# Kernel tuning notes

Hardware: AMD Instinct MI355X
Metric: run time of the kernel (lower is better)

The kernel has to match this reference:

```python
import jax, jax.numpy as jnp
import numpy as np

S, B, D = 2048, 4, 512
H, R, QK, FFN = 8, 8, 32, 2048
HD = D // H  # 64


def _ln(x, g, b, eps=1e-5):
    mu = jnp.mean(x, axis=-1, keepdims=True)
    var = jnp.var(x, axis=-1, keepdims=True)
    return (x - mu) * jax.lax.rsqrt(var + eps) * g + b


def setup_inputs() -> dict:
    key = jax.random.key(0)
    ks = jax.random.split(key, 16)
    w = lambda k, shape: (jax.random.normal(k, shape, jnp.float32) * 0.02)
    return {
        "x": jax.random.normal(ks[0], (S, B, D), jnp.float32),
        "Wq": w(ks[1], (D, D)),        "bq": jnp.zeros((D,), jnp.float32),
        "Wk": w(ks[2], (D, D)),        "bk": jnp.zeros((D,), jnp.float32),
        "Wv": w(ks[3], (D, HD * R)),   "bv": jnp.zeros((HD * R,), jnp.float32),
        "Wqv": w(ks[4], (D, QK * H)),  "bqv": jnp.zeros((QK * H,), jnp.float32),
        "Wkv": w(ks[5], (HD, QK)),     "bkv": jnp.zeros((QK,), jnp.float32),
        "Wf": w(ks[6], (D, D)),        "bf": jnp.zeros((D,), jnp.float32),
        "W1": w(ks[7], (D, FFN)),      "b1": jnp.zeros((FFN,), jnp.float32),
        "W2": w(ks[8], (FFN, D)),      "b2": jnp.zeros((D,), jnp.float32),
        "g1": jnp.ones((D,), jnp.float32),  "be1": jnp.zeros((D,), jnp.float32),
        "g2": jnp.ones((D,), jnp.float32),  "be2": jnp.zeros((D,), jnp.float32),
    }


def reference(x, Wq, bq, Wk, bk, Wv, bv, Wqv, bqv, Wkv, bkv, Wf, bf,
              W1, b1, W2, b2, g1, be1, g2, be2):
    # x: [S, B, D] -> [B, S, D]
    xb = jnp.transpose(x, (1, 0, 2))
    bsz, n, _ = xb.shape
    res = xb

    # stage 1: per-head attention over positions
    q = (xb @ Wq + bq).reshape(bsz, n, H, HD) / np.sqrt(HD).astype(np.float32)
    k = (xb @ Wk + bk).reshape(bsz, n, H, HD)
    v = (xb @ Wv + bv).reshape(bsz, n, R, HD)
    score = jax.nn.softmax(jnp.einsum("bshd,bthd->bhst", q, k), axis=-1)  # [B,H,S,S]
    # retrieved values per (head, rule): [B, S, H, R, HD]
    out = jnp.einsum("bhst,btrd->bshrd", score, v)

    # stage 2: composition softmax over rules
    qv = (xb @ Wqv + bqv).reshape(bsz, n, H, QK) / np.sqrt(QK).astype(np.float32)
    kv = out @ Wkv + bkv  # [B,S,H,R,QK]
    comp = jax.nn.softmax(jnp.einsum("bshq,bshrq->bshr", qv, kv), axis=-1)
    o = jnp.einsum("bshr,bshrd->bshd", comp, out).reshape(bsz, n, D)
    o = o @ Wf + bf

    # post-norm residual + FFN (norm_before=False)
    o = _ln(res + o, g1, be1)
    ffn = jax.nn.relu(o @ W1 + b1) @ W2 + b2
    o = _ln(o + ffn, g2, be2)
    return jnp.transpose(o, (1, 0, 2))  # back to [S, B, D]
```

## Files before the change

### kernel.cpp

```cpp
#include <hip/hip_runtime.h>
#include <hip/hip_bf16.h>

typedef __bf16 bf16;
typedef bf16 bf16x4 __attribute__((ext_vector_type(4)));
typedef bf16 bf16x8 __attribute__((ext_vector_type(8)));
typedef float f32x4 __attribute__((ext_vector_type(4)));

constexpr int SEQ  = 2048;
constexpr int BAT  = 4;
constexpr int NH   = 8;
constexpr int NTOK = SEQ * BAT;
constexpr int QKVW = 1792;
constexpr size_t MB = 1ull << 20;

__device__ inline void async_lds16(const void* g, void* l) {
  __builtin_amdgcn_global_load_lds(
      (__attribute__((address_space(1))) void*)(g),
      (__attribute__((address_space(3))) void*)(l), 16, 0, 0);
}

#define MFMA16 __builtin_amdgcn_mfma_f32_16x16x32_bf16

__global__ __launch_bounds__(512)
void attn_kernel(const bf16* __restrict__ qkv, const bf16* __restrict__ vT,
                 bf16* __restrict__ outb) {
  __shared__ __align__(16) bf16 Qs[64 * 64];
  __shared__ __align__(16) bf16 Ks[2][128 * 64];
  __shared__ __align__(16) bf16 Ps[64 * 128];
  __shared__ float rsAll[8][64];
  __shared__ float rsInv[64];

  const int tid = threadIdx.x;
  const int lane = tid & 63, w = tid >> 6;
  const int r16 = lane & 15, rq = lane >> 4;
  const int qb = blockIdx.x, h = blockIdx.y, b = blockIdx.z;

  const bf16* qbase = qkv + ((long)b * SEQ + qb * 64) * QKVW + h * 64;
  {
    const int rr = tid >> 3, sl = tid & 7;
    async_lds16(qbase + (long)rr * QKVW + ((sl ^ (rr & 7)) << 3),
                Qs + (size_t)w * 512);
  }
  const bf16* kbase = qkv + (long)b * SEQ * QKVW + 512 + h * 64;
  auto stageK = [&](int buf, int t0) {
#pragma unroll
    for (int g = 0; g < 2; g++) {
      const int c = g * 512 + tid;
      const int rr = c >> 3, sl = c & 7;
      async_lds16(kbase + (long)(t0 + rr) * QKVW + ((sl ^ (rr & 7)) << 3),
                  Ks[buf] + (size_t)(g * 8 + w) * 512);
    }
  };
  const bf16* vp[4];
#pragma unroll
  for (int n = 0; n < 4; n++)
    vp[n] = vT + ((long)b * 512 + w * 64 + n * 16 + r16) * SEQ + rq * 8;

  f32x4 acc[4][4] = {};
  float rs[4] = {};

  stageK(0, 0);
  asm volatile("s_waitcnt vmcnt(0)" ::: "memory");
  __builtin_amdgcn_s_barrier();
  __builtin_amdgcn_sched_barrier(0);

  bf16x8 qf[4][2];
#pragma unroll
  for (int j = 0; j < 4; j++)
#pragma unroll
    for (int kf = 0; kf < 2; kf++) {
      const int row = j * 16 + r16;
      qf[j][kf] = *(const bf16x8*)&Qs[row * 64 + (((kf * 4 + rq) ^ (row & 7)) << 3)];
    }

  const int krow = w * 16 + r16;
  for (int t = 0; t < 16; ++t) {
    const int t0 = t * 128;
    if (t) {
      asm volatile("s_waitcnt vmcnt(0)" ::: "memory");
      __builtin_amdgcn_s_barrier();
      __builtin_amdgcn_sched_barrier(0);
    }
    if (t < 15) stageK((t + 1) & 1, t0 + 128);
    bf16x8 va0 = *(const bf16x8*)(vp[0] + t0);
    bf16x8 va1 = *(const bf16x8*)(vp[1] + t0);
    bf16x8 va2 = *(const bf16x8*)(vp[2] + t0);
    bf16x8 va3 = *(const bf16x8*)(vp[3] + t0);
    bf16x8 kfr[2];
#pragma unroll
    for (int kf = 0; kf < 2; kf++)
      kfr[kf] = *(const bf16x8*)&Ks[t & 1][krow * 64 + (((kf * 4 + rq) ^ (krow & 7)) << 3)];
    f32x4 s[4] = {};
#pragma unroll
    for (int j = 0; j < 4; j++) {
      s[j] = MFMA16(kfr[0], qf[j][0], s[j], 0, 0, 0);
      s[j] = MFMA16(kfr[1], qf[j][1], s[j], 0, 0, 0);
    }
#pragma unroll
    for (int j = 0; j < 4; j++) {
      const float e0 = __expf(s[j][0]), e1 = __expf(s[j][1]);
      const float e2 = __expf(s[j][2]), e3 = __expf(s[j][3]);
      rs[j] += (e0 + e1) + (e2 + e3);
      bf16x4 pk; pk[0] = (bf16)e0; pk[1] = (bf16)e1; pk[2] = (bf16)e2; pk[3] = (bf16)e3;
      const int row = j * 16 + r16;
      *(bf16x4*)&Ps[row * 128 + (((w * 2 + (rq >> 1)) ^ (row & 7)) << 3) + ((rq & 1) << 2)] = pk;
    }
    asm volatile("s_waitcnt lgkmcnt(0)" ::: "memory");
    __builtin_amdgcn_s_barrier();
    __builtin_amdgcn_sched_barrier(0);
    bf16x8 pf[4];
#pragma unroll
    for (int i = 0; i < 4; i++) {
      const int row = i * 16 + r16;
      pf[i] = *(const bf16x8*)&Ps[row * 128 + (((rq + 0) ^ (row & 7)) << 3)];
    }
    bf16x8 vb0 = *(const bf16x8*)(vp[0] + t0 + 32);
    bf16x8 vb1 = *(const bf16x8*)(vp[1] + t0 + 32);
    bf16x8 vb2 = *(const bf16x8*)(vp[2] + t0 + 32);
    bf16x8 vb3 = *(const bf16x8*)(vp[3] + t0 + 32);
#pragma unroll
    for (int i = 0; i < 4; i++) {
      acc[i][0] = MFMA16(pf[i], va0, acc[i][0], 0, 0, 0);
      acc[i][1] = MFMA16(pf[i], va1, acc[i][1], 0, 0, 0);
      acc[i][2] = MFMA16(pf[i], va2, acc[i][2], 0, 0, 0);
      acc[i][3] = MFMA16(pf[i], va3, acc[i][3], 0, 0, 0);
    }
#pragma unroll
    for (int i = 0; i < 4; i++) {
      const int row = i * 16 + r16;
      pf[i] = *(const bf16x8*)&Ps[row * 128 + (((rq + 4) ^ (row & 7)) << 3)];
    }
    va0 = *(const bf16x8*)(vp[0] + t0 + 64);
    va1 = *(const bf16x8*)(vp[1] + t0 + 64);
    va2 = *(const bf16x8*)(vp[2] + t0 + 64);
    va3 = *(const bf16x8*)(vp[3] + t0 + 64);
#pragma unroll
    for (int i = 0; i < 4; i++) {
      acc[i][0] = MFMA16(pf[i], vb0, acc[i][0], 0, 0, 0);
      acc[i][1] = MFMA16(pf[i], vb1, acc[i][1], 0, 0, 0);
      acc[i][2] = MFMA16(pf[i], vb2, acc[i][2], 0, 0, 0);
      acc[i][3] = MFMA16(pf[i], vb3, acc[i][3], 0, 0, 0);
    }
#pragma unroll
    for (int i = 0; i < 4; i++) {
      const int row = i * 16 + r16;
      pf[i] = *(const bf16x8*)&Ps[row * 128 + (((rq + 8) ^ (row & 7)) << 3)];
    }
    vb0 = *(const bf16x8*)(vp[0] + t0 + 96);
    vb1 = *(const bf16x8*)(vp[1] + t0 + 96);
    vb2 = *(const bf16x8*)(vp[2] + t0 + 96);
    vb3 = *(const bf16x8*)(vp[3] + t0 + 96);
#pragma unroll
    for (int i = 0; i < 4; i++) {
      acc[i][0] = MFMA16(pf[i], va0, acc[i][0], 0, 0, 0);
      acc[i][1] = MFMA16(pf[i], va1, acc[i][1], 0, 0, 0);
      acc[i][2] = MFMA16(pf[i], va2, acc[i][2], 0, 0, 0);
      acc[i][3] = MFMA16(pf[i], va3, acc[i][3], 0, 0, 0);
    }
#pragma unroll
    for (int i = 0; i < 4; i++) {
      const int row = i * 16 + r16;
      pf[i] = *(const bf16x8*)&Ps[row * 128 + (((rq + 12) ^ (row & 7)) << 3)];
    }
#pragma unroll
    for (int i = 0; i < 4; i++) {
      acc[i][0] = MFMA16(pf[i], vb0, acc[i][0], 0, 0, 0);
      acc[i][1] = MFMA16(pf[i], vb1, acc[i][1], 0, 0, 0);
      acc[i][2] = MFMA16(pf[i], vb2, acc[i][2], 0, 0, 0);
      acc[i][3] = MFMA16(pf[i], vb3, acc[i][3], 0, 0, 0);
    }
    __builtin_amdgcn_s_barrier();
  }

#pragma unroll
  for (int j = 0; j < 4; j++) {
    rs[j] += __shfl_xor(rs[j], 16);
    rs[j] += __shfl_xor(rs[j], 32);
  }
  if (rq == 0) {
#pragma unroll
    for (int j = 0; j < 4; j++) rsAll[w][j * 16 + r16] = rs[j];
  }
  asm volatile("s_waitcnt lgkmcnt(0)" ::: "memory");
  __builtin_amdgcn_s_barrier();
  if (tid < 64) {
    float tot = 0.f;
#pragma unroll
    for (int u = 0; u < 8; u++) tot += rsAll[u][tid];
    rsInv[tid] = 1.f / tot;
  }
  asm volatile("s_waitcnt lgkmcnt(0)" ::: "memory");
  __builtin_amdgcn_s_barrier();

  bf16* obase = outb + (((long)(b * NH + h) * SEQ) + qb * 64) * 512 + w * 64;
#pragma unroll
  for (int i = 0; i < 4; i++) {
#pragma unroll
    for (int rg = 0; rg < 4; rg++) {
      const int row = i * 16 + rq * 4 + rg;
      const float inv = rsInv[row];
#pragma unroll
      for (int n = 0; n < 4; n++)
        obase[(long)row * 512 + n * 16 + r16] = (bf16)(acc[i][n][rg] * inv);
    }
  }
}

__global__ __launch_bounds__(256)
void gemm_bt(const bf16* __restrict__ A, const bf16* __restrict__ B,
             void* __restrict__ C, const float* __restrict__ bias,
             int K, int lda, int ldb, int ldc,
             long sAz, long sBz, long sCz,
             float scale, int flags) {
  constexpr int LPT = 4;
  __shared__ __align__(16) bf16 As[3][128 * 32];
  __shared__ __align__(16) bf16 Bs[3][128 * 32];

  const int tid  = threadIdx.x;
  const int lane = tid & 63;
  const int w    = tid >> 6;
  const int wr   = w >> 1, wc = w & 1;

  const int gx = gridDim.x, gy = gridDim.y;
  const int nwg = gx * gy * gridDim.z;
  const int flat = blockIdx.x + gx * (blockIdx.y + gy * blockIdx.z);
  const int q = nwg >> 3, r = nwg & 7;
  const int xcd = flat & 7, pos = flat >> 3;
  int swz = (xcd < r ? xcd * (q + 1) : r * (q + 1) + (xcd - r) * q) + pos;
  const int bx = swz % gx; swz /= gx;
  const int by = swz % gy;
  const long z = swz / gy;

  const bf16* Ab = A + (long)by * 128 * lda + z * sAz;
  const bf16* Bb = B + (long)bx * 128 * ldb + z * sBz;

  const bf16* aSrc[2];
  const bf16* bSrc[2];
#pragma unroll
  for (int g = 0; g < 2; g++) {
    const int c = (w * 2 + g) * 64 + lane;
    const int rr = c >> 2, sl = c & 3;
    aSrc[g] = Ab + (long)rr * lda + ((sl ^ ((rr >> 1) & 3)) << 3);
    bSrc[g] = Bb + (long)rr * ldb + ((sl ^ ((rr >> 1) & 3)) << 3);
  }

  f32x4 acc[4][4] = {};
  const int r16 = lane & 15, kq = lane >> 4;
  const int so = ((kq ^ ((r16 >> 1) & 3)) << 3);

  auto stage = [&](int buf, int k0) {
#pragma unroll
    for (int g = 0; g < 2; g++)
      async_lds16(aSrc[g] + k0, &As[buf][(w * 2 + g) * 512]);
#pragma unroll
    for (int g = 0; g < 2; g++)
      async_lds16(bSrc[g] + k0, &Bs[buf][(w * 2 + g) * 512]);
  };
  bf16x8 areg[4], breg[4];
  auto loadfrags = [&](int buf) {
#pragma unroll
    for (int i = 0; i < 4; i++)
      areg[i] = *(const bf16x8*)&As[buf][(wr * 64 + i * 16 + r16) * 32 + so];
#pragma unroll
    for (int j = 0; j < 4; j++)
      breg[j] = *(const bf16x8*)&Bs[buf][(wc * 64 + j * 16 + r16) * 32 + so];
  };
  auto domfma = [&]() {
    __builtin_amdgcn_s_setprio(1);
#pragma unroll
    for (int i = 0; i < 4; i++)
#pragma unroll
      for (int j = 0; j < 4; j++)
        acc[i][j] = MFMA16(areg[i], breg[j], acc[i][j], 0, 0, 0);
    __builtin_amdgcn_s_setprio(0);
  };

  const int nt = K >> 5;
  stage(0, 0);
  if (nt > 1) stage(1, 32);

  int cs = 2, cc = 0;
  for (int t = 0; t + 2 < nt; ++t) {
    stage(cs, (t + 2) * 32);
    asm volatile("s_waitcnt vmcnt(%0)" : : "n"(2 * LPT) : "memory");
    __builtin_amdgcn_s_barrier();
    loadfrags(cc);
    asm volatile("s_waitcnt lgkmcnt(0)" : : : "memory");
    __builtin_amdgcn_sched_barrier(0);
    __builtin_amdgcn_s_barrier();
    domfma();
    if (++cs == 3) cs = 0;
    if (++cc == 3) cc = 0;
  }
  if (nt >= 2) {
    asm volatile("s_waitcnt vmcnt(%0)" : : "n"(LPT) : "memory");
    __builtin_amdgcn_s_barrier();
    loadfrags(cc);
    asm volatile("s_waitcnt lgkmcnt(0)" : : : "memory");
    __builtin_amdgcn_sched_barrier(0);
    domfma();
    if (++cc == 3) cc = 0;
  }
  asm volatile("s_waitcnt vmcnt(0)" : : : "memory");
  __builtin_amdgcn_s_barrier();
  loadfrags(cc);
  domfma();

  const long rowBase = (long)by * 128 + wr * 64;
  const int  colBase = bx * 128 + wc * 64;
  float* Cf = (float*)C;
  bf16*  Cb = (bf16*)C;
  const int rq = lane >> 4;
#pragma unroll
  for (int i = 0; i < 4; i++) {
#pragma unroll
    for (int j = 0; j < 4; j++) {
      const int col = colBase + j * 16 + r16;
      const float bv = (bias && z == 0) ? bias[col] : 0.f;
#pragma unroll
      for (int rg = 0; rg < 4; rg++) {
        const long row = rowBase + i * 16 + rq * 4 + rg;
        float y = (acc[i][j][rg] + bv) * scale;
        if (flags & 2) y = fmaxf(y, 0.f);
        const long idx = z * sCz + row * (long)ldc + col;
        if (flags & 1) Cb[idx] = (bf16)y;
        else           Cf[idx] = y;
      }
    }
  }
}

__global__ void transpose_w_kernel(const float* __restrict__ in, bf16* __restrict__ out,
                                   int K, int N, float scale) {
  __shared__ float t[32][33];
  const int n0 = blockIdx.x * 32, k0 = blockIdx.y * 32;
  const int tx = threadIdx.x, ty = threadIdx.y;
#pragma unroll
  for (int i = ty; i < 32; i += 8)
    t[i][tx] = in[(long)(k0 + i) * N + n0 + tx];
  __syncthreads();
#pragma unroll
  for (int i = ty; i < 32; i += 8)
    out[(long)(n0 + i) * K + k0 + tx] = (bf16)(t[tx][i] * scale);
}

__global__ void build_bias_kernel(const float* bq, const float* bk,
                                  const float* bv, const float* bqv,
                                  float* __restrict__ out) {
  const int i = blockIdx.x * 256 + threadIdx.x;
  float v;
  if (i < 512)       v = bq[i] * 0.125f;
  else if (i < 1024) v = bk[i - 512];
  else if (i < 1536) v = bv[i - 1024];
  else               v = bqv[i - 1536] * 0.17677669529663687f;
  out[i] = v;
}

__global__ void transpose_v_kernel(const bf16* __restrict__ qkv, bf16* __restrict__ vT) {
  __shared__ bf16 t[32][33];
  const int s0 = blockIdx.x * 32, c0 = blockIdx.y * 32, b = blockIdx.z;
  const int tx = threadIdx.x, ty = threadIdx.y;
#pragma unroll
  for (int i = ty; i < 32; i += 8)
    t[i][tx] = qkv[((long)b * SEQ + s0 + i) * QKVW + 1024 + c0 + tx];
  __syncthreads();
#pragma unroll
  for (int i = ty; i < 32; i += 8)
    vT[(long)b * 512 * SEQ + (long)(c0 + i) * SEQ + s0 + tx] = t[tx][i];
}

__global__ __launch_bounds__(256)
void convert_x_kernel(const float* __restrict__ x, bf16* __restrict__ xb) {
  const long i0 = ((long)blockIdx.x * 256 + threadIdx.x) * 8;
  const int t = (int)(i0 >> 9), d = (int)(i0 & 511);
  const int b = t >> 11, s = t & 2047;
  const float* src = x + ((long)(s * BAT + b) << 9) + d;
  const float4 f0 = *(const float4*)(src);
  const float4 f1 = *(const float4*)(src + 4);
  bf16x8 o;
  o[0] = (bf16)f0.x; o[1] = (bf16)f0.y; o[2] = (bf16)f0.z; o[3] = (bf16)f0.w;
  o[4] = (bf16)f1.x; o[5] = (bf16)f1.y; o[6] = (bf16)f1.z; o[7] = (bf16)f1.w;
  *(bf16x8*)&xb[i0] = o;
}

__global__ __launch_bounds__(256)
void stage2_kernel(const bf16* __restrict__ outbuf, long strideB,
                   const bf16* __restrict__ qvb, int qvStride,
                   const float* __restrict__ Wkv,
                   const float* __restrict__ bkv,
                   bf16* __restrict__ attn) {
  const int lane = threadIdx.x & 63, wid = threadIdx.x >> 6;
  const int g = blockIdx.x * 4 + wid;
  const int s = g & 2047, h = (g >> 11) & 7, b = g >> 14;
  const int token = b * SEQ + s;

  const bf16* qv = qvb + (long)token * qvStride + h * 32;
  const float* wrow = Wkv + lane * 32;
  float wq = 0.f, cb = 0.f;
#pragma unroll 8
  for (int q = 0; q < 32; q++) {
    const float qf = (float)qv[q];
    wq += wrow[q] * qf;
    cb += bkv[q] * qf;
  }

  const bf16* orow = outbuf + b * strideB + ((long)(h << 11) + s) * 512;
  float of[8], lg[8];
#pragma unroll
  for (int r = 0; r < 8; r++) {
    of[r] = (float)orow[r * 64 + lane];
    float p = of[r] * wq;
    for (int o = 1; o < 64; o <<= 1) p += __shfl_xor(p, o);
    lg[r] = p + cb;
  }
  float m = lg[0];
#pragma unroll
  for (int r = 1; r < 8; r++) m = fmaxf(m, lg[r]);
  float e[8], sum = 0.f;
#pragma unroll
  for (int r = 0; r < 8; r++) { e[r] = __expf(lg[r] - m); sum += e[r]; }
  const float inv = 1.f / sum;
  float o = 0.f;
#pragma unroll
  for (int r = 0; r < 8; r++) o += e[r] * inv * of[r];
  attn[(long)token * 512 + h * 64 + lane] = (bf16)o;
}

__global__ __launch_bounds__(256)
void ln_kernel(const float* __restrict__ a, long part2,
               const float* __restrict__ bres, int bresT,
               const float* __restrict__ g, const float* __restrict__ be,
               float* __restrict__ outF, bf16* __restrict__ outB, int outT) {
  __shared__ float red[8];
  const int t = blockIdx.x, tid = threadIdx.x;
  const int b = t >> 11, s = t & 2047;
  const long ti = (long)t * 512;
  const long xi = (long)(s * BAT + b) * 512;
  const long ri = bresT ? xi : ti;
  float v0 = a[ti + tid]       + bres[ri + tid];
  float v1 = a[ti + 256 + tid] + bres[ri + 256 + tid];
  if (part2) { v0 += a[part2 + ti + tid]; v1 += a[part2 + ti + 256 + tid]; }
  float sum = v0 + v1, sq = v0 * v0 + v1 * v1;
  const int lane = tid & 63, wid = tid >> 6;
  for (int o = 1; o < 64; o <<= 1) { sum += __shfl_xor(sum, o); sq += __shfl_xor(sq, o); }
  if (lane == 0) { red[wid] = sum; red[4 + wid] = sq; }
  __syncthreads();
  sum = red[0] + red[1] + red[2] + red[3];
  sq  = red[4] + red[5] + red[6] + red[7];
  const float mu = sum * (1.f / 512.f);
  const float var = sq * (1.f / 512.f) - mu * mu;
  const float rs = rsqrtf(var + 1e-5f);
  const float y0 = (v0 - mu) * rs * g[tid] + be[tid];
  const float y1 = (v1 - mu) * rs * g[tid + 256] + be[tid + 256];
  const long oi = outT ? xi : ti;
  if (outF) { outF[oi + tid] = y0; outF[oi + 256 + tid] = y1; }
  if (outB) { outB[ti + tid] = (bf16)y0; outB[ti + 256 + tid] = (bf16)y1; }
}

extern "C" void kernel_launch(void* const* d_in, const int* in_sizes, int n_in,
                              void* d_out, int out_size, void* d_ws, size_t ws_size,
                              hipStream_t stream) {
  const float* x   = (const float*)d_in[0];
  const float* Wq  = (const float*)d_in[1];
  const float* bq  = (const float*)d_in[2];
  const float* Wk  = (const float*)d_in[3];
  const float* bk  = (const float*)d_in[4];
  const float* Wv  = (const float*)d_in[5];
  const float* bv  = (const float*)d_in[6];
  const float* Wqv = (const float*)d_in[7];
  const float* bqv = (const float*)d_in[8];
  const float* Wkv = (const float*)d_in[9];
  const float* bkv = (const float*)d_in[10];
  const float* Wf  = (const float*)d_in[11];
  const float* bfc = (const float*)d_in[12];
  const float* W1  = (const float*)d_in[13];
  const float* b1  = (const float*)d_in[14];
  const float* W2  = (const float*)d_in[15];
  const float* b2  = (const float*)d_in[16];
  const float* g1  = (const float*)d_in[17];
  const float* be1 = (const float*)d_in[18];
  const float* g2  = (const float*)d_in[19];
  const float* be2 = (const float*)d_in[20];

  char* ws = (char*)d_ws;
  size_t off = 0;
  auto alloc = [&](size_t bytes) -> void* {
    void* p = ws + off;
    off += (bytes + 1023) & ~(size_t)1023;
    return p;
  };
  bf16*  qkv   = (bf16*)alloc((size_t)NTOK * QKVW * 2);
  bf16*  vT    = (bf16*)alloc((size_t)BAT * 512 * SEQ * 2);
  bf16*  wtPk  = (bf16*)alloc((size_t)QKVW * 512 * 2);
  bf16*  WfT   = (bf16*)alloc(512 * 512 * 2);
  bf16*  W1T   = (bf16*)alloc((size_t)2048 * 512 * 2);
  bf16*  W2T   = (bf16*)alloc((size_t)512 * 2048 * 2);
  float* bcat  = (float*)alloc(QKVW * 4);
  bf16*  attn  = (bf16*)alloc((size_t)NTOK * 512 * 2);

  char* reg = ws + off;
  bf16*  outb  = (bf16*)reg;
  bf16*  xb    = (bf16*)reg;
  float* wfoP  = (float*)(reg + 8 * MB);
  float* ln1f  = (float*)(reg + 40 * MB);
  bf16*  ln1b  = (bf16*)(reg + 56 * MB);
  bf16*  ffn1  = (bf16*)(reg + 64 * MB);

  const dim3 tb(32, 8);
  transpose_w_kernel<<<dim3(16, 16), tb, 0, stream>>>(Wq,  wtPk,              512, 512, 0.125f);
  transpose_w_kernel<<<dim3(16, 16), tb, 0, stream>>>(Wk,  wtPk + 512  * 512, 512, 512, 1.f);
  transpose_w_kernel<<<dim3(16, 16), tb, 0, stream>>>(Wv,  wtPk + 1024 * 512, 512, 512, 1.f);
  transpose_w_kernel<<<dim3(8, 16),  tb, 0, stream>>>(Wqv, wtPk + 1536 * 512, 512, 256, 0.17677669529663687f);
  transpose_w_kernel<<<dim3(16, 16), tb, 0, stream>>>(Wf,  WfT, 512, 512, 1.f);
  transpose_w_kernel<<<dim3(64, 16), tb, 0, stream>>>(W1,  W1T, 512, 2048, 1.f);
  transpose_w_kernel<<<dim3(16, 64), tb, 0, stream>>>(W2,  W2T, 2048, 512, 1.f);
  build_bias_kernel<<<7, 256, 0, stream>>>(bq, bk, bv, bqv, bcat);
  convert_x_kernel<<<2048, 256, 0, stream>>>(x, xb);

  gemm_bt<<<dim3(14, 64, 1), 256, 0, stream>>>(xb, wtPk, qkv, bcat,
      512, 512, 512, QKVW, 0, 0, 0, 1.f, 1);

  transpose_v_kernel<<<dim3(64, 16, 4), tb, 0, stream>>>(qkv, vT);

  attn_kernel<<<dim3(SEQ / 64, NH, BAT), 512, 0, stream>>>(qkv, vT, outb);

  stage2_kernel<<<BAT * NH * SEQ / 4, 256, 0, stream>>>(outb, (long)NH * SEQ * 512,
      qkv + 1536, QKVW, Wkv, bkv, attn);

  const long sWf = (long)NTOK * 512;
  gemm_bt<<<dim3(4, 64, 2), 256, 0, stream>>>(attn, WfT, wfoP, bfc,
      256, 512, 512, 512, 256, 256, sWf, 1.f, 0);
  ln_kernel<<<NTOK, 256, 0, stream>>>(wfoP, sWf, x, 1, g1, be1, ln1f, ln1b, 0);
  gemm_bt<<<dim3(16, 64, 1), 256, 0, stream>>>(ln1b, W1T, ffn1, b1,
      512, 512, 512, 2048, 0, 0, 0, 1.f, 1 | 2);
  gemm_bt<<<dim3(4, 64, 2), 256, 0, stream>>>(ffn1, W2T, wfoP, b2,
      1024, 2048, 2048, 512, 1024, 1024, sWf, 1.f, 0);
  ln_kernel<<<NTOK, 256, 0, stream>>>(wfoP, sWf, ln1f, 0, g2, be2, (float*)d_out, nullptr, 1);
}
```

Before: 549.4 us.

## Double-buffer P tile, prefetch all V fragments upfront, and swizzle block order

The P tile in shared memory is now double-buffered. This removes the trailing barrier at the end of each key-tile iteration. All 16 V-fragment global loads for the tile are issued at the start of the iteration, ahead of the QK MFMAs, so their latency overlaps with the score computation. Block indices are also remapped with a swizzle so that consecutive workgroups land on different (head, batch) slices, aiming for better L2 locality across the XCDs. In exchange the kernel uses more LDS and more VGPRs for the held V fragments, which may lower occupancy.

Result: slower. 595.6 us (+8.4%).

```diff
diff --git a/kernel.cpp b/kernel.cpp
--- a/kernel.cpp
+++ b/kernel.cpp
@@ -26,14 +26,17 @@
                  bf16* __restrict__ outb) {
   __shared__ __align__(16) bf16 Qs[64 * 64];
   __shared__ __align__(16) bf16 Ks[2][128 * 64];
-  __shared__ __align__(16) bf16 Ps[64 * 128];
+  __shared__ __align__(16) bf16 Ps[2][64 * 128];
   __shared__ float rsAll[8][64];
   __shared__ float rsInv[64];
 
   const int tid = threadIdx.x;
   const int lane = tid & 63, w = tid >> 6;
   const int r16 = lane & 15, rq = lane >> 4;
-  const int qb = blockIdx.x, h = blockIdx.y, b = blockIdx.z;
+
+  const int flat = blockIdx.x + 32 * (blockIdx.y + 8 * blockIdx.z);
+  const int swz = (flat & 7) * 128 + (flat >> 3);
+  const int qb = swz & 31, h = (swz >> 5) & 7, b = swz >> 8;
 
   const bf16* qbase = qkv + ((long)b * SEQ + qb * 64) * QKVW + h * 64;
   {
@@ -82,10 +85,13 @@
       __builtin_amdgcn_sched_barrier(0);
     }
     if (t < 15) stageK((t + 1) & 1, t0 + 128);
-    bf16x8 va0 = *(const bf16x8*)(vp[0] + t0);
-    bf16x8 va1 = *(const bf16x8*)(vp[1] + t0);
-    bf16x8 va2 = *(const bf16x8*)(vp[2] + t0);
-    bf16x8 va3 = *(const bf16x8*)(vp[3] + t0);
+    bf16x8 vv[16];
+#pragma unroll
+    for (int c = 0; c < 4; c++)
+#pragma unroll
+      for (int n = 0; n < 4; n++)
+        vv[c * 4 + n] = *(const bf16x8*)(vp[n] + t0 + c * 32);
+    __builtin_amdgcn_sched_barrier(0);
     bf16x8 kfr[2];
 #pragma unroll
     for (int kf = 0; kf < 2; kf++)
@@ -96,6 +102,7 @@
       s[j] = MFMA16(kfr[0], qf[j][0], s[j], 0, 0, 0);
       s[j] = MFMA16(kfr[1], qf[j][1], s[j], 0, 0, 0);
     }
+    bf16* Pcur = Ps[t & 1];
 #pragma unroll
     for (int j = 0; j < 4; j++) {
       const float e0 = __expf(s[j][0]), e1 = __expf(s[j][1]);
@@ -103,73 +110,27 @@
       rs[j] += (e0 + e1) + (e2 + e3);
       bf16x4 pk; pk[0] = (bf16)e0; pk[1] = (bf16)e1; pk[2] = (bf16)e2; pk[3] = (bf16)e3;
       const int row = j * 16 + r16;
-      *(bf16x4*)&Ps[row * 128 + (((w * 2 + (rq >> 1)) ^ (row & 7)) << 3) + ((rq & 1) << 2)] = pk;
+      *(bf16x4*)&Pcur[row * 128 + (((w * 2 + (rq >> 1)) ^ (row & 7)) << 3) + ((rq & 1) << 2)] = pk;
     }
     asm volatile("s_waitcnt lgkmcnt(0)" ::: "memory");
     __builtin_amdgcn_s_barrier();
     __builtin_amdgcn_sched_barrier(0);
-    bf16x8 pf[4];
-#pragma unroll
-    for (int i = 0; i < 4; i++) {
-      const int row = i * 16 + r16;
-      pf[i] = *(const bf16x8*)&Ps[row * 128 + (((rq + 0) ^ (row & 7)) << 3)];
-    }
-    bf16x8 vb0 = *(const bf16x8*)(vp[0] + t0 + 32);
-    bf16x8 vb1 = *(const bf16x8*)(vp[1] + t0 + 32);
-    bf16x8 vb2 = *(const bf16x8*)(vp[2] + t0 + 32);
-    bf16x8 vb3 = *(const bf16x8*)(vp[3] + t0 + 32);
-#pragma unroll
-    for (int i = 0; i < 4; i++) {
-      acc[i][0] = MFMA16(pf[i], va0, acc[i][0], 0, 0, 0);
-      acc[i][1] = MFMA16(pf[i], va1, acc[i][1], 0, 0, 0);
-      acc[i][2] = MFMA16(pf[i], va2, acc[i][2], 0, 0, 0);
-      acc[i][3] = MFMA16(pf[i], va3, acc[i][3], 0, 0, 0);
-    }
-#pragma unroll
-    for (int i = 0; i < 4; i++) {
-      const int row = i * 16 + r16;
-      pf[i] = *(const bf16x8*)&Ps[row * 128 + (((rq + 4) ^ (row & 7)) << 3)];
-    }
-    va0 = *(const bf16x8*)(vp[0] + t0 + 64);
-    va1 = *(const bf16x8*)(vp[1] + t0 + 64);
-    va2 = *(const bf16x8*)(vp[2] + t0 + 64);
-    va3 = *(const bf16x8*)(vp[3] + t0 + 64);
-#pragma unroll
-    for (int i = 0; i < 4; i++) {
-      acc[i][0] = MFMA16(pf[i], vb0, acc[i][0], 0, 0, 0);
-      acc[i][1] = MFMA16(pf[i], vb1, acc[i][1], 0, 0, 0);
-      acc[i][2] = MFMA16(pf[i], vb2, acc[i][2], 0, 0, 0);
-      acc[i][3] = MFMA16(pf[i], vb3, acc[i][3], 0, 0, 0);
-    }
-#pragma unroll
-    for (int i = 0; i < 4; i++) {
-      const int row = i * 16 + r16;
-      pf[i] = *(const bf16x8*)&Ps[row * 128 + (((rq + 8) ^ (row & 7)) << 3)];
-    }
-    vb0 = *(const bf16x8*)(vp[0] + t0 + 96);
-    vb1 = *(const bf16x8*)(vp[1] + t0 + 96);
-    vb2 = *(const bf16x8*)(vp[2] + t0 + 96);
-    vb3 = *(const bf16x8*)(vp[3] + t0 + 96);
-#pragma unroll
-    for (int i = 0; i < 4; i++) {
-      acc[i][0] = MFMA16(pf[i], va0, acc[i][0], 0, 0, 0);
-      acc[i][1] = MFMA16(pf[i], va1, acc[i][1], 0, 0, 0);
-      acc[i][2] = MFMA16(pf[i], va2, acc[i][2], 0, 0, 0);
-      acc[i][3] = MFMA16(pf[i], va3, acc[i][3], 0, 0, 0);
-    }
-#pragma unroll
-    for (int i = 0; i < 4; i++) {
-      const int row = i * 16 + r16;
-      pf[i] = *(const bf16x8*)&Ps[row * 128 + (((rq + 12) ^ (row & 7)) << 3)];
-    }
-#pragma unroll
-    for (int i = 0; i < 4; i++) {
-      acc[i][0] = MFMA16(pf[i], vb0, acc[i][0], 0, 0, 0);
-      acc[i][1] = MFMA16(pf[i], vb1, acc[i][1], 0, 0, 0);
-      acc[i][2] = MFMA16(pf[i], vb2, acc[i][2], 0, 0, 0);
-      acc[i][3] = MFMA16(pf[i], vb3, acc[i][3], 0, 0, 0);
-    }
-    __builtin_amdgcn_s_barrier();
+#pragma unroll
+    for (int c = 0; c < 4; c++) {
+      bf16x8 pf[4];
+#pragma unroll
+      for (int i = 0; i < 4; i++) {
+        const int row = i * 16 + r16;
+        pf[i] = *(const bf16x8*)&Pcur[row * 128 + (((rq + c * 4) ^ (row & 7)) << 3)];
+      }
+#pragma unroll
+      for (int i = 0; i < 4; i++) {
+        acc[i][0] = MFMA16(pf[i], vv[c * 4 + 0], acc[i][0], 0, 0, 0);
+        acc[i][1] = MFMA16(pf[i], vv[c * 4 + 1], acc[i][1], 0, 0, 0);
+        acc[i][2] = MFMA16(pf[i], vv[c * 4 + 2], acc[i][2], 0, 0, 0);
+        acc[i][3] = MFMA16(pf[i], vv[c * 4 + 3], acc[i][3], 0, 0, 0);
+      }
+    }
   }
 
 #pragma unroll
```
